# Kernel tuning notes

Hardware: AMD Instinct MI355X
Metric: run time of the kernel (lower is better)

The kernel has to match this reference:

```python
import jax, jax.numpy as jnp
import numpy as np

D_KEY = 128

def setup_inputs() -> dict:
    key = jax.random.key(0)
    k1, k2, k3, k4 = jax.random.split(key, 4)
    B, S, D = 4, 4096, 1024
    inp = jax.random.normal(k1, (B, S, D), dtype=jnp.float32)
    # torch Linear weight layout: [out_features, in_features]
    Wq = jax.random.normal(k2, (D_KEY, D), dtype=jnp.float32) / np.sqrt(D)
    Wk = jax.random.normal(k3, (D_KEY, D), dtype=jnp.float32) / np.sqrt(D)
    Wv = jax.random.normal(k4, (D_KEY, D), dtype=jnp.float32) / np.sqrt(D)
    # causal mask: 0 => masked out (matches masked_fill(mask == 0, -inf))
    mask = jnp.tril(jnp.ones((S, S), dtype=jnp.int32))
    return {"input": inp, "Wq": Wq, "Wk": Wk, "Wv": Wv, "mask": mask}

def reference(input, Wq, Wk, Wv, mask):
    # projections (no bias, eval mode -> no weight noise)
    q = jnp.einsum('bsd,kd->bsk', input, Wq)  # [B,S,d_key]
    k = jnp.einsum('bsd,kd->bsk', input, Wk)
    v = jnp.einsum('bsd,kd->bsk', input, Wv)
    attn = jnp.einsum('bqk,bsk->bqs', q, k)   # [B,S,S]
    attn = jnp.where(mask == 0, -jnp.inf, attn)
    scale = np.float32(np.sqrt(D_KEY))
    p = jax.nn.softmax(attn / scale, axis=-1)
    return jnp.einsum('bqs,bsk->bqk', p, v)   # [B,S,d_key]
```

## Files before the change

### kernel.cpp

```cpp
#include <hip/hip_runtime.h>
#include <hip/hip_bf16.h>

typedef __bf16 bf16_t;
typedef bf16_t bf16x8 __attribute__((ext_vector_type(8)));
typedef bf16_t bf16x4 __attribute__((ext_vector_type(4)));
typedef float  f32x4  __attribute__((ext_vector_type(4)));

#define LOG2E    1.4426950408889634f
#define QK_SCALE 0.08838834764831845f

static constexpr int BB = 4, SS = 4096, DD = 1024, DK = 128;

static constexpr size_t WB_OFF = 0;
static constexpr size_t Q_OFF  = 1u << 20;
static constexpr size_t K_OFF  = Q_OFF + (size_t)BB * SS * DK * 2;
static constexpr size_t VT_OFF = K_OFF + (size_t)BB * SS * DK * 2;

__global__ __launch_bounds__(256) void wconv_kernel(const float* __restrict__ Wq,
                                                    const float* __restrict__ Wk,
                                                    const float* __restrict__ Wv,
                                                    bf16_t* __restrict__ wb) {
    int i4 = blockIdx.x * 256 + threadIdx.x;
    int e  = i4 * 4;
    const float* src = (e < 131072) ? Wq : (e < 262144 ? Wk : Wv);
    float scale = (e < 131072) ? (QK_SCALE * LOG2E) : 1.0f;
    int off = e & 131071;
    f32x4 v = *(const f32x4*)(src + off);
    bf16x4 o = { (bf16_t)(v[0] * scale), (bf16_t)(v[1] * scale),
                 (bf16_t)(v[2] * scale), (bf16_t)(v[3] * scale) };
    *(bf16x4*)(wb + e) = o;
}

__global__ __launch_bounds__(256) void proj_kernel(const float* __restrict__ inp,
                                                   const bf16_t* __restrict__ wb,
                                                   bf16_t* __restrict__ qo,
                                                   bf16_t* __restrict__ ko,
                                                   bf16_t* __restrict__ vto) {
    __shared__ bf16_t At[64][72];
    __shared__ bf16_t Wt[128][72];

    const int tid = threadIdx.x;
    const int w = tid >> 6, lane = tid & 63;
    const int lr = lane & 15, lh = lane >> 4;
    const int wr = w >> 1, wc = w & 1;
    const int m0 = blockIdx.x * 64;
    const int y  = blockIdx.y;

    f32x4  aReg[4];
    bf16x8 wReg[4];

    auto LOAD = [&](int k0) {
        #pragma unroll
        for (int i = 0; i < 4; ++i) {
            int u = tid + i * 256;
            aReg[i] = *(const f32x4*)(inp + (size_t)(m0 + (u >> 4)) * DD + k0 + (u & 15) * 4);
        }
        #pragma unroll
        for (int i = 0; i < 4; ++i) {
            int u = tid + i * 256;
            wReg[i] = *(const bf16x8*)(wb + (size_t)(y * 128 + (u >> 3)) * DD + k0 + (u & 7) * 8);
        }
    };

    LOAD(0);
    f32x4 acc[2][4] = {};

    for (int k0 = 0; k0 < DD; k0 += 64) {
        if (k0) __syncthreads();
        #pragma unroll
        for (int i = 0; i < 4; ++i) {
            int u = tid + i * 256;
            bf16x4 bv = { (bf16_t)aReg[i][0], (bf16_t)aReg[i][1],
                          (bf16_t)aReg[i][2], (bf16_t)aReg[i][3] };
            *(bf16x4*)&At[u >> 4][(u & 15) * 4] = bv;
        }
        #pragma unroll
        for (int i = 0; i < 4; ++i) {
            int u = tid + i * 256;
            *(bf16x8*)&Wt[u >> 3][(u & 7) * 8] = wReg[i];
        }
        __syncthreads();
        if (k0 + 64 < DD) LOAD(k0 + 64);
        #pragma unroll
        for (int kk = 0; kk < 64; kk += 32) {
            bf16x8 a0 = *(const bf16x8*)&At[wr * 32      + lr][kk + lh * 8];
            bf16x8 a1 = *(const bf16x8*)&At[wr * 32 + 16 + lr][kk + lh * 8];
            #pragma unroll
            for (int ct = 0; ct < 4; ++ct) {
                bf16x8 wf = *(const bf16x8*)&Wt[wc * 64 + ct * 16 + lr][kk + lh * 8];
                acc[0][ct] = __builtin_amdgcn_mfma_f32_16x16x32_bf16(a0, wf, acc[0][ct], 0, 0, 0);
                acc[1][ct] = __builtin_amdgcn_mfma_f32_16x16x32_bf16(a1, wf, acc[1][ct], 0, 0, 0);
            }
        }
    }

    if (y < 2) {
        bf16_t* out = (y == 0) ? qo : ko;
        #pragma unroll
        for (int rt = 0; rt < 2; ++rt)
            #pragma unroll
            for (int ct = 0; ct < 4; ++ct)
                #pragma unroll
                for (int r = 0; r < 4; ++r) {
                    int m = m0 + wr * 32 + rt * 16 + lh * 4 + r;
                    out[(size_t)m * DK + wc * 64 + ct * 16 + lr] = (bf16_t)acc[rt][ct][r];
                }
    } else {
        int b = m0 >> 12;
        int sbase = (m0 & 4095) + wr * 32;
        #pragma unroll
        for (int rt = 0; rt < 2; ++rt)
            #pragma unroll
            for (int ct = 0; ct < 4; ++ct) {
                bf16x4 pk = { (bf16_t)acc[rt][ct][0], (bf16_t)acc[rt][ct][1],
                              (bf16_t)acc[rt][ct][2], (bf16_t)acc[rt][ct][3] };
                int s = sbase + rt * 16 + lh * 4;
                int d = wc * 64 + ct * 16 + lr;
                *(bf16x4*)(vto + (size_t)b * DK * SS + (size_t)d * SS + s) = pk;
            }
    }
}

__global__ __launch_bounds__(256) void attn_kernel(const bf16_t* __restrict__ q,
                                                   const bf16_t* __restrict__ k,
                                                   const bf16_t* __restrict__ vt,
                                                   float* __restrict__ out) {
    __shared__ bf16_t Pl[4][16][72];
    __shared__ float  ml[4][16][2];
    __shared__ float  Osh[16][128];

    const int tid = threadIdx.x, w = tid >> 6, lane = tid & 63;
    const int lr = lane & 15, lh = lane >> 4;
    const int bid = blockIdx.x;
    const int b = bid >> 8;
    const int i = bid & 255;
    int t;
    if      (b == 0) t = i;
    else if (b == 1) t = 255 - i;
    else if (b == 2) t = (i + 128) & 255;
    else             t = (383 - i) & 255;
    const int q0 = t * 16;
    const int NT = t / 4 + 1;

    const bf16_t* qb = q  + (size_t)b * SS * DK;
    const bf16_t* kb = k  + (size_t)b * SS * DK;
    const bf16_t* vb = vt + (size_t)b * DK * SS;

    bf16x8 qf[4];
    #pragma unroll
    for (int kc = 0; kc < 4; ++kc)
        qf[kc] = *(const bf16x8*)(qb + (size_t)(q0 + lr) * DK + kc * 32 + lh * 8);

    f32x4 oacc[8] = {};
    float mv[4], lv[4];
    #pragma unroll
    for (int r = 0; r < 4; ++r) { mv[r] = -INFINITY; lv[r] = 0.f; }

    for (int kt = w; kt < NT; kt += 4) {
        const int kvb = kt * 64;
        f32x4 sf[4] = {};
        #pragma unroll
        for (int ct = 0; ct < 4; ++ct) {
            bf16x8 kf[4];
            #pragma unroll
            for (int kc = 0; kc < 4; ++kc)
                kf[kc] = *(const bf16x8*)(kb + (size_t)(kvb + ct * 16 + lr) * DK + kc * 32 + lh * 8);
            #pragma unroll
            for (int kc = 0; kc < 4; ++kc)
                sf[ct] = __builtin_amdgcn_mfma_f32_16x16x32_bf16(qf[kc], kf[kc], sf[ct], 0, 0, 0);
        }
        const bool need_mask = (kvb + 63 > q0);
        float alpha[4];
        #pragma unroll
        for (int r = 0; r < 4; ++r) {
            float vals[4];
            float mx = -INFINITY;
            #pragma unroll
            for (int ct = 0; ct < 4; ++ct) {
                float v = sf[ct][r];
                if (need_mask) {
                    int kv_g = kvb + ct * 16 + lr;
                    int q_g  = q0 + lh * 4 + r;
                    if (kv_g > q_g) v = -INFINITY;
                }
                vals[ct] = v;
                mx = fmaxf(mx, v);
            }
            mx = fmaxf(mx, __shfl_xor(mx, 1));
            mx = fmaxf(mx, __shfl_xor(mx, 2));
            mx = fmaxf(mx, __shfl_xor(mx, 4));
            mx = fmaxf(mx, __shfl_xor(mx, 8));
            float mnew = fmaxf(mv[r], mx);
            float al   = exp2f(mv[r] - mnew);
            mv[r]  = mnew;
            float rs = 0.f;
            #pragma unroll
            for (int ct = 0; ct < 4; ++ct) {
                float p = exp2f(vals[ct] - mnew);
                rs += p;
                Pl[w][lh * 4 + r][ct * 16 + lr] = (bf16_t)p;
            }
            rs += __shfl_xor(rs, 1);
            rs += __shfl_xor(rs, 2);
            rs += __shfl_xor(rs, 4);
            rs += __shfl_xor(rs, 8);
            lv[r] = lv[r] * al + rs;
            alpha[r] = al;
        }
        #pragma unroll
        for (int dt = 0; dt < 8; ++dt)
            #pragma unroll
            for (int r = 0; r < 4; ++r)
                oacc[dt][r] *= alpha[r];
        bf16x8 pa[2];
        #pragma unroll
        for (int kc = 0; kc < 2; ++kc)
            pa[kc] = *(const bf16x8*)&Pl[w][lr][kc * 32 + lh * 8];
        #pragma unroll
        for (int dt = 0; dt < 8; ++dt) {
            const bf16_t* vrow = vb + (size_t)(dt * 16 + lr) * SS + kvb + lh * 8;
            bf16x8 vf0 = *(const bf16x8*)(vrow);
            bf16x8 vf1 = *(const bf16x8*)(vrow + 32);
            oacc[dt] = __builtin_amdgcn_mfma_f32_16x16x32_bf16(pa[0], vf0, oacc[dt], 0, 0, 0);
            oacc[dt] = __builtin_amdgcn_mfma_f32_16x16x32_bf16(pa[1], vf1, oacc[dt], 0, 0, 0);
        }
    }

    if (lr == 0) {
        #pragma unroll
        for (int r = 0; r < 4; ++r) {
            int row = lh * 4 + r;
            ml[w][row][0] = mv[r];
            ml[w][row][1] = lv[r];
        }
    }
    #pragma unroll
    for (int i2 = 0; i2 < 2; ++i2) {
        int u = tid + i2 * 256;
        *(f32x4*)&Osh[u >> 5][(u & 31) * 4] = f32x4{0.f, 0.f, 0.f, 0.f};
    }
    __syncthreads();
    #pragma unroll
    for (int r = 0; r < 4; ++r) {
        int row = lh * 4 + r;
        float M = ml[0][row][0];
        #pragma unroll
        for (int ww = 1; ww < 4; ++ww) M = fmaxf(M, ml[ww][row][0]);
        float sc = exp2f(mv[r] - M);
        #pragma unroll
        for (int dt = 0; dt < 8; ++dt)
            atomicAdd(&Osh[row][dt * 16 + lr], oacc[dt][r] * sc);
    }
    __syncthreads();
    float* ob = out + ((size_t)b * SS + q0) * DK;
    #pragma unroll
    for (int i2 = 0; i2 < 2; ++i2) {
        int u = tid + i2 * 256;
        int row = u >> 5, c = (u & 31) * 4;
        float M = ml[0][row][0];
        #pragma unroll
        for (int ww = 1; ww < 4; ++ww) M = fmaxf(M, ml[ww][row][0]);
        float L = 0.f;
        #pragma unroll
        for (int ww = 0; ww < 4; ++ww)
            L = fmaf(ml[ww][row][1], exp2f(ml[ww][row][0] - M), L);
        f32x4 o = *(const f32x4*)&Osh[row][c];
        f32x4 res = { o[0] / L, o[1] / L, o[2] / L, o[3] / L };
        *(f32x4*)(ob + (size_t)row * DK + c) = res;
    }
}

extern "C" void kernel_launch(void* const* d_in, const int* in_sizes, int n_in,
                              void* d_out, int out_size, void* d_ws, size_t ws_size,
                              hipStream_t stream) {
    const float* inp = (const float*)d_in[0];
    const float* Wq  = (const float*)d_in[1];
    const float* Wk  = (const float*)d_in[2];
    const float* Wv  = (const float*)d_in[3];

    char* ws = (char*)d_ws;
    bf16_t* wb  = (bf16_t*)(ws + WB_OFF);
    bf16_t* qw  = (bf16_t*)(ws + Q_OFF);
    bf16_t* kw  = (bf16_t*)(ws + K_OFF);
    bf16_t* vtw = (bf16_t*)(ws + VT_OFF);
    float*  o   = (float*)d_out;

    wconv_kernel<<<384, 256, 0, stream>>>(Wq, Wk, Wv, wb);
    proj_kernel<<<dim3(256, 3), 256, 0, stream>>>(inp, wb, qw, kw, vtw);
    attn_kernel<<<1024, 256, 0, stream>>>(qw, kw, vtw, o);
}
```

Baseline: 367.5 us.

## Pair low/high causal query tiles per block to share K/V loads

The attention kernel now gives each block two 16-row query tiles, j and 255-j. Each K tile is loaded once and multiplied against both query tiles, and the V tile is shared the same way. This balances causal work across blocks and halves the K/V traffic for the overlapping range. The S tile is computed transposed (K as the A operand) so each lane owns one query row, which removes the cross-row shuffles in softmax. The projection kernel tile drops from 64 to 32 rows with twice the blocks. The cost is more registers per thread (two accumulator sets), which may lower occupancy.

```diff
diff --git a/kernel.cpp b/kernel.cpp
--- a/kernel.cpp
+++ b/kernel.cpp
@@ -36,22 +36,21 @@
                                                    bf16_t* __restrict__ qo,
                                                    bf16_t* __restrict__ ko,
                                                    bf16_t* __restrict__ vto) {
-    __shared__ bf16_t At[64][72];
+    __shared__ bf16_t At[32][72];
     __shared__ bf16_t Wt[128][72];
 
     const int tid = threadIdx.x;
     const int w = tid >> 6, lane = tid & 63;
     const int lr = lane & 15, lh = lane >> 4;
-    const int wr = w >> 1, wc = w & 1;
-    const int m0 = blockIdx.x * 64;
+    const int wr = (w >> 1) * 16, wc = (w & 1) * 64;
+    const int m0 = blockIdx.x * 32;
     const int y  = blockIdx.y;
 
-    f32x4  aReg[4];
+    f32x4  aReg[2];
     bf16x8 wReg[4];
-
     auto LOAD = [&](int k0) {
         #pragma unroll
-        for (int i = 0; i < 4; ++i) {
+        for (int i = 0; i < 2; ++i) {
             int u = tid + i * 256;
             aReg[i] = *(const f32x4*)(inp + (size_t)(m0 + (u >> 4)) * DD + k0 + (u & 15) * 4);
         }
@@ -63,12 +62,12 @@
     };
 
     LOAD(0);
-    f32x4 acc[2][4] = {};
+    f32x4 acc[4] = {};
 
     for (int k0 = 0; k0 < DD; k0 += 64) {
         if (k0) __syncthreads();
         #pragma unroll
-        for (int i = 0; i < 4; ++i) {
+        for (int i = 0; i < 2; ++i) {
             int u = tid + i * 256;
             bf16x4 bv = { (bf16_t)aReg[i][0], (bf16_t)aReg[i][1],
                           (bf16_t)aReg[i][2], (bf16_t)aReg[i][3] };
@@ -83,13 +82,11 @@
         if (k0 + 64 < DD) LOAD(k0 + 64);
         #pragma unroll
         for (int kk = 0; kk < 64; kk += 32) {
-            bf16x8 a0 = *(const bf16x8*)&At[wr * 32      + lr][kk + lh * 8];
-            bf16x8 a1 = *(const bf16x8*)&At[wr * 32 + 16 + lr][kk + lh * 8];
+            bf16x8 a = *(const bf16x8*)&At[wr + lr][kk + lh * 8];
             #pragma unroll
             for (int ct = 0; ct < 4; ++ct) {
-                bf16x8 wf = *(const bf16x8*)&Wt[wc * 64 + ct * 16 + lr][kk + lh * 8];
-                acc[0][ct] = __builtin_amdgcn_mfma_f32_16x16x32_bf16(a0, wf, acc[0][ct], 0, 0, 0);
-                acc[1][ct] = __builtin_amdgcn_mfma_f32_16x16x32_bf16(a1, wf, acc[1][ct], 0, 0, 0);
+                bf16x8 wf = *(const bf16x8*)&Wt[wc + ct * 16 + lr][kk + lh * 8];
+                acc[ct] = __builtin_amdgcn_mfma_f32_16x16x32_bf16(a, wf, acc[ct], 0, 0, 0);
             }
         }
     }
@@ -97,68 +94,102 @@
     if (y < 2) {
         bf16_t* out = (y == 0) ? qo : ko;
         #pragma unroll
-        for (int rt = 0; rt < 2; ++rt)
-            #pragma unroll
-            for (int ct = 0; ct < 4; ++ct)
-                #pragma unroll
-                for (int r = 0; r < 4; ++r) {
-                    int m = m0 + wr * 32 + rt * 16 + lh * 4 + r;
-                    out[(size_t)m * DK + wc * 64 + ct * 16 + lr] = (bf16_t)acc[rt][ct][r];
-                }
+        for (int ct = 0; ct < 4; ++ct)
+            #pragma unroll
+            for (int r = 0; r < 4; ++r) {
+                int m = m0 + wr + lh * 4 + r;
+                out[(size_t)m * DK + wc + ct * 16 + lr] = (bf16_t)acc[ct][r];
+            }
     } else {
-        int b = m0 >> 12;
-        int sbase = (m0 & 4095) + wr * 32;
-        #pragma unroll
-        for (int rt = 0; rt < 2; ++rt)
-            #pragma unroll
-            for (int ct = 0; ct < 4; ++ct) {
-                bf16x4 pk = { (bf16_t)acc[rt][ct][0], (bf16_t)acc[rt][ct][1],
-                              (bf16_t)acc[rt][ct][2], (bf16_t)acc[rt][ct][3] };
-                int s = sbase + rt * 16 + lh * 4;
-                int d = wc * 64 + ct * 16 + lr;
-                *(bf16x4*)(vto + (size_t)b * DK * SS + (size_t)d * SS + s) = pk;
-            }
-    }
+        int b = m0 >> 12, sbase = (m0 & 4095) + wr;
+        #pragma unroll
+        for (int ct = 0; ct < 4; ++ct) {
+            bf16x4 pk = { (bf16_t)acc[ct][0], (bf16_t)acc[ct][1],
+                          (bf16_t)acc[ct][2], (bf16_t)acc[ct][3] };
+            int s = sbase + lh * 4;
+            int d = wc + ct * 16 + lr;
+            *(bf16x4*)(vto + (size_t)b * DK * SS + (size_t)d * SS + s) = pk;
+        }
+    }
+}
+
+__device__ __forceinline__ void softmax16(f32x4 (&sf)[4], float& mv, float& lv,
+                                          f32x4 (&oacc)[8], bf16_t* Prow,
+                                          int qg, int kvb, bool msk, int lr, int lh) {
+    if (msk) {
+        #pragma unroll
+        for (int ct = 0; ct < 4; ++ct)
+            #pragma unroll
+            for (int r = 0; r < 4; ++r) {
+                int kv_g = kvb + ct * 16 + lh * 4 + r;
+                if (kv_g > qg + lr) sf[ct][r] = -INFINITY;
+            }
+    }
+    float mx = -INFINITY;
+    #pragma unroll
+    for (int ct = 0; ct < 4; ++ct)
+        #pragma unroll
+        for (int r = 0; r < 4; ++r) mx = fmaxf(mx, sf[ct][r]);
+    mx = fmaxf(mx, __shfl_xor(mx, 16));
+    mx = fmaxf(mx, __shfl_xor(mx, 32));
+    float mnew = fmaxf(mv, mx);
+    float al   = exp2f(mv - mnew);
+    mv = mnew;
+    float rs = 0.f;
+    #pragma unroll
+    for (int ct = 0; ct < 4; ++ct) {
+        float p0 = exp2f(sf[ct][0] - mnew);
+        float p1 = exp2f(sf[ct][1] - mnew);
+        float p2 = exp2f(sf[ct][2] - mnew);
+        float p3 = exp2f(sf[ct][3] - mnew);
+        rs += (p0 + p1) + (p2 + p3);
+        bf16x4 pk = { (bf16_t)p0, (bf16_t)p1, (bf16_t)p2, (bf16_t)p3 };
+        *(bf16x4*)(Prow + ct * 16 + lh * 4) = pk;
+    }
+    rs += __shfl_xor(rs, 16);
+    rs += __shfl_xor(rs, 32);
+    lv = lv * al + rs;
+    #pragma unroll
+    for (int dt = 0; dt < 8; ++dt) oacc[dt] *= al;
 }
 
 __global__ __launch_bounds__(256) void attn_kernel(const bf16_t* __restrict__ q,
                                                    const bf16_t* __restrict__ k,
                                                    const bf16_t* __restrict__ vt,
                                                    float* __restrict__ out) {
-    __shared__ bf16_t Pl[4][16][72];
-    __shared__ float  ml[4][16][2];
-    __shared__ float  Osh[16][128];
+    __shared__ bf16_t Pl[4][2][16][72];
+    __shared__ float  ml[4][32][2];
+    __shared__ float  Osh[32][132];
 
     const int tid = threadIdx.x, w = tid >> 6, lane = tid & 63;
     const int lr = lane & 15, lh = lane >> 4;
-    const int bid = blockIdx.x;
-    const int b = bid >> 8;
-    const int i = bid & 255;
-    int t;
-    if      (b == 0) t = i;
-    else if (b == 1) t = 255 - i;
-    else if (b == 2) t = (i + 128) & 255;
-    else             t = (383 - i) & 255;
-    const int q0 = t * 16;
-    const int NT = t / 4 + 1;
+    const int b  = blockIdx.x >> 7;
+    const int j  = blockIdx.x & 127;
+    const int q_lo = j * 16;
+    const int q_hi = (255 - j) * 16;
+    const int NT = q_hi / 64 + 1;
 
     const bf16_t* qb = q  + (size_t)b * SS * DK;
     const bf16_t* kb = k  + (size_t)b * SS * DK;
     const bf16_t* vb = vt + (size_t)b * DK * SS;
 
-    bf16x8 qf[4];
-    #pragma unroll
-    for (int kc = 0; kc < 4; ++kc)
-        qf[kc] = *(const bf16x8*)(qb + (size_t)(q0 + lr) * DK + kc * 32 + lh * 8);
-
-    f32x4 oacc[8] = {};
-    float mv[4], lv[4];
-    #pragma unroll
-    for (int r = 0; r < 4; ++r) { mv[r] = -INFINITY; lv[r] = 0.f; }
+    bf16x8 qf0[4], qf1[4];
+    #pragma unroll
+    for (int kc = 0; kc < 4; ++kc) {
+        qf0[kc] = *(const bf16x8*)(qb + (size_t)(q_lo + lr) * DK + kc * 32 + lh * 8);
+        qf1[kc] = *(const bf16x8*)(qb + (size_t)(q_hi + lr) * DK + kc * 32 + lh * 8);
+    }
+
+    f32x4 oacc0[8] = {}, oacc1[8] = {};
+    float mv0 = -INFINITY, mv1 = -INFINITY, lv0 = 0.f, lv1 = 0.f;
+
+    bf16_t* Prow0 = &Pl[w][0][lr][0];
+    bf16_t* Prow1 = &Pl[w][1][lr][0];
 
     for (int kt = w; kt < NT; kt += 4) {
         const int kvb = kt * 64;
-        f32x4 sf[4] = {};
+        const bool lo = (kvb <= q_lo + 15);
+        f32x4 sf1[4] = {}, sf0[4] = {};
         #pragma unroll
         for (int ct = 0; ct < 4; ++ct) {
             bf16x8 kf[4];
@@ -167,106 +198,92 @@
                 kf[kc] = *(const bf16x8*)(kb + (size_t)(kvb + ct * 16 + lr) * DK + kc * 32 + lh * 8);
             #pragma unroll
             for (int kc = 0; kc < 4; ++kc)
-                sf[ct] = __builtin_amdgcn_mfma_f32_16x16x32_bf16(qf[kc], kf[kc], sf[ct], 0, 0, 0);
-        }
-        const bool need_mask = (kvb + 63 > q0);
-        float alpha[4];
-        #pragma unroll
-        for (int r = 0; r < 4; ++r) {
-            float vals[4];
-            float mx = -INFINITY;
-            #pragma unroll
-            for (int ct = 0; ct < 4; ++ct) {
-                float v = sf[ct][r];
-                if (need_mask) {
-                    int kv_g = kvb + ct * 16 + lr;
-                    int q_g  = q0 + lh * 4 + r;
-                    if (kv_g > q_g) v = -INFINITY;
-                }
-                vals[ct] = v;
-                mx = fmaxf(mx, v);
-            }
-            mx = fmaxf(mx, __shfl_xor(mx, 1));
-            mx = fmaxf(mx, __shfl_xor(mx, 2));
-            mx = fmaxf(mx, __shfl_xor(mx, 4));
-            mx = fmaxf(mx, __shfl_xor(mx, 8));
-            float mnew = fmaxf(mv[r], mx);
-            float al   = exp2f(mv[r] - mnew);
-            mv[r]  = mnew;
-            float rs = 0.f;
-            #pragma unroll
-            for (int ct = 0; ct < 4; ++ct) {
-                float p = exp2f(vals[ct] - mnew);
-                rs += p;
-                Pl[w][lh * 4 + r][ct * 16 + lr] = (bf16_t)p;
-            }
-            rs += __shfl_xor(rs, 1);
-            rs += __shfl_xor(rs, 2);
-            rs += __shfl_xor(rs, 4);
-            rs += __shfl_xor(rs, 8);
-            lv[r] = lv[r] * al + rs;
-            alpha[r] = al;
-        }
-        #pragma unroll
-        for (int dt = 0; dt < 8; ++dt)
-            #pragma unroll
-            for (int r = 0; r < 4; ++r)
-                oacc[dt][r] *= alpha[r];
-        bf16x8 pa[2];
-        #pragma unroll
-        for (int kc = 0; kc < 2; ++kc)
-            pa[kc] = *(const bf16x8*)&Pl[w][lr][kc * 32 + lh * 8];
+                sf1[ct] = __builtin_amdgcn_mfma_f32_16x16x32_bf16(kf[kc], qf1[kc], sf1[ct], 0, 0, 0);
+            if (lo) {
+                #pragma unroll
+                for (int kc = 0; kc < 4; ++kc)
+                    sf0[ct] = __builtin_amdgcn_mfma_f32_16x16x32_bf16(kf[kc], qf0[kc], sf0[ct], 0, 0, 0);
+            }
+        }
+        softmax16(sf1, mv1, lv1, oacc1, Prow1, q_hi, kvb, kvb + 63 > q_hi, lr, lh);
+        if (lo) softmax16(sf0, mv0, lv0, oacc0, Prow0, q_lo, kvb, kvb + 63 > q_lo, lr, lh);
+
+        asm volatile("" ::: "memory");
+
+        bf16x8 pa1[2], pa0[2];
+        #pragma unroll
+        for (int kc = 0; kc < 2; ++kc) {
+            bf16x4 plo = *(const bf16x4*)(Prow1 + kc * 32 + lh * 8);
+            bf16x4 phi = *(const bf16x4*)(Prow1 + kc * 32 + lh * 8 + 4);
+            pa1[kc] = __builtin_shufflevector(plo, phi, 0, 1, 2, 3, 4, 5, 6, 7);
+        }
+        if (lo) {
+            #pragma unroll
+            for (int kc = 0; kc < 2; ++kc) {
+                bf16x4 plo = *(const bf16x4*)(Prow0 + kc * 32 + lh * 8);
+                bf16x4 phi = *(const bf16x4*)(Prow0 + kc * 32 + lh * 8 + 4);
+                pa0[kc] = __builtin_shufflevector(plo, phi, 0, 1, 2, 3, 4, 5, 6, 7);
+            }
+        }
         #pragma unroll
         for (int dt = 0; dt < 8; ++dt) {
             const bf16_t* vrow = vb + (size_t)(dt * 16 + lr) * SS + kvb + lh * 8;
             bf16x8 vf0 = *(const bf16x8*)(vrow);
             bf16x8 vf1 = *(const bf16x8*)(vrow + 32);
-            oacc[dt] = __builtin_amdgcn_mfma_f32_16x16x32_bf16(pa[0], vf0, oacc[dt], 0, 0, 0);
-            oacc[dt] = __builtin_amdgcn_mfma_f32_16x16x32_bf16(pa[1], vf1, oacc[dt], 0, 0, 0);
-        }
-    }
-
-    if (lr == 0) {
-        #pragma unroll
-        for (int r = 0; r < 4; ++r) {
-            int row = lh * 4 + r;
-            ml[w][row][0] = mv[r];
-            ml[w][row][1] = lv[r];
-        }
-    }
-    #pragma unroll
-    for (int i2 = 0; i2 < 2; ++i2) {
-        int u = tid + i2 * 256;
-        *(f32x4*)&Osh[u >> 5][(u & 31) * 4] = f32x4{0.f, 0.f, 0.f, 0.f};
-    }
+            oacc1[dt] = __builtin_amdgcn_mfma_f32_16x16x32_bf16(vf0, pa1[0], oacc1[dt], 0, 0, 0);
+            oacc1[dt] = __builtin_amdgcn_mfma_f32_16x16x32_bf16(vf1, pa1[1], oacc1[dt], 0, 0, 0);
+            if (lo) {
+                oacc0[dt] = __builtin_amdgcn_mfma_f32_16x16x32_bf16(vf0, pa0[0], oacc0[dt], 0, 0, 0);
+                oacc0[dt] = __builtin_amdgcn_mfma_f32_16x16x32_bf16(vf1, pa0[1], oacc0[dt], 0, 0, 0);
+            }
+        }
+        asm volatile("" ::: "memory");
+    }
+
+    if (lh == 0) {
+        ml[w][lr][0]      = mv0;  ml[w][lr][1]      = lv0;
+        ml[w][16 + lr][0] = mv1;  ml[w][16 + lr][1] = lv1;
+    }
+    float* osh1 = &Osh[0][0];
+    for (int u = tid; u < 32 * 132; u += 256) osh1[u] = 0.f;
     __syncthreads();
-    #pragma unroll
-    for (int r = 0; r < 4; ++r) {
-        int row = lh * 4 + r;
-        float M = ml[0][row][0];
-        #pragma unroll
-        for (int ww = 1; ww < 4; ++ww) M = fmaxf(M, ml[ww][row][0]);
-        float sc = exp2f(mv[r] - M);
+    {
+        int row = lr;
+        float M = fmaxf(fmaxf(ml[0][row][0], ml[1][row][0]),
+                        fmaxf(ml[2][row][0], ml[3][row][0]));
+        float sc = exp2f(mv0 - M);
         #pragma unroll
         for (int dt = 0; dt < 8; ++dt)
-            atomicAdd(&Osh[row][dt * 16 + lr], oacc[dt][r] * sc);
+            #pragma unroll
+            for (int r = 0; r < 4; ++r)
+                atomicAdd(&Osh[row][dt * 16 + lh * 4 + r], oacc0[dt][r] * sc);
+    }
+    {
+        int row = 16 + lr;
+        float M = fmaxf(fmaxf(ml[0][row][0], ml[1][row][0]),
+                        fmaxf(ml[2][row][0], ml[3][row][0]));
+        float sc = exp2f(mv1 - M);
+        #pragma unroll
+        for (int dt = 0; dt < 8; ++dt)
+            #pragma unroll
+            for (int r = 0; r < 4; ++r)
+                atomicAdd(&Osh[row][dt * 16 + lh * 4 + r], oacc1[dt][r] * sc);
     }
     __syncthreads();
-    float* ob = out + ((size_t)b * SS + q0) * DK;
-    #pragma unroll
-    for (int i2 = 0; i2 < 2; ++i2) {
+    #pragma unroll
+    for (int i2 = 0; i2 < 4; ++i2) {
         int u = tid + i2 * 256;
         int row = u >> 5, c = (u & 31) * 4;
-        float M = ml[0][row][0];
-        #pragma unroll
-        for (int ww = 1; ww < 4; ++ww) M = fmaxf(M, ml[ww][row][0]);
+        float M = fmaxf(fmaxf(ml[0][row][0], ml[1][row][0]),
+                        fmaxf(ml[2][row][0], ml[3][row][0]));
         float L = 0.f;
         #pragma unroll
         for (int ww = 0; ww < 4; ++ww)
             L = fmaf(ml[ww][row][1], exp2f(ml[ww][row][0] - M), L);
         f32x4 o = *(const f32x4*)&Osh[row][c];
         f32x4 res = { o[0] / L, o[1] / L, o[2] / L, o[3] / L };
-        *(f32x4*)(ob + (size_t)row * DK + c) = res;
+        int qg = (row < 16) ? (q_lo + row) : (q_hi + row - 16);
+        *(f32x4*)(out + ((size_t)b * SS + qg) * DK + c) = res;
     }
 }
 
@@ -286,6 +303,6 @@
     float*  o   = (float*)d_out;
 
     wconv_kernel<<<384, 256, 0, stream>>>(Wq, Wk, Wv, wb);
-    proj_kernel<<<dim3(256, 3), 256, 0, stream>>>(inp, wb, qw, kw, vtw);
-    attn_kernel<<<1024, 256, 0, stream>>>(qw, kw, vtw, o);
-}
+    proj_kernel<<<dim3(512, 3), 256, 0, stream>>>(inp, wb, qw, kw, vtw);
+    attn_kernel<<<512, 256, 0, stream>>>(qw, kw, vtw, o);
+}
```

After: 376.7 us. +2.5%, slower.
